# Kernel optimization log

Measured on AMD Instinct MI355X. Metric: run time of the kernel, lower is better.

The kernel has to match this reference:

```python
import jax, jax.numpy as jnp
import numpy as np

B, L, C, H = 4, 2048, 1024, 16
D = C // H            # head_dim = 64
HALF = D // 2         # 32
MAX_SCALE_MUL = float(np.log(100.0))


def setup_inputs() -> dict:
    key = jax.random.key(0)
    ks = jax.random.split(key, 6)
    x = jax.random.normal(ks[0], (B, L, C), dtype=jnp.float32)
    # causal additive bias [1,1,L,L]
    causal = jnp.tril(jnp.ones((L, L), dtype=bool))
    attn_bias = jnp.where(causal, 0.0, -1e9).astype(jnp.float32)[None, None]
    # RoPE cos/sin table: [B, 2, L, half]
    inv_freq = 1.0 / (10000.0 ** (jnp.arange(HALF, dtype=jnp.float32) / HALF))
    ang = jnp.arange(L, dtype=jnp.float32)[:, None] * inv_freq[None, :]  # [L, half]
    rope = jnp.stack([jnp.cos(ang), jnp.sin(ang)], axis=0)               # [2, L, half]
    rope_batch = jnp.broadcast_to(rope[None], (B, 2, L, HALF)).astype(jnp.float32)
    mat_qkv_w = jax.random.normal(ks[1], (3 * C, C), dtype=jnp.float32) * (1.0 / np.sqrt(C))
    q_bias = jnp.zeros((C,), dtype=jnp.float32)
    v_bias = jnp.zeros((C,), dtype=jnp.float32)
    proj_w = jax.random.normal(ks[2], (C, C), dtype=jnp.float32) * (1.0 / np.sqrt(C))
    proj_b = jnp.zeros((C,), dtype=jnp.float32)
    scale_mul = jnp.full((1, H, 1, 1), np.log(4.0), dtype=jnp.float32)
    return {"x": x, "attn_bias": attn_bias, "rope_batch": rope_batch,
            "mat_qkv_w": mat_qkv_w, "q_bias": q_bias, "v_bias": v_bias,
            "proj_w": proj_w, "proj_b": proj_b, "scale_mul": scale_mul}


def _l2norm(t, eps=1e-12):
    # F.normalize(t, dim=-1)
    n = jnp.sqrt(jnp.sum(t * t, axis=-1, keepdims=True))
    return t / jnp.maximum(n, eps)


def reference(x, attn_bias, rope_batch, mat_qkv_w, q_bias, v_bias, proj_w, proj_b, scale_mul):
    b, l, c = x.shape
    bias_cat = jnp.concatenate([q_bias, jnp.zeros_like(q_bias), v_bias])  # [3C]
    qkv = (x @ mat_qkv_w.T + bias_cat).reshape(b, l, 3, H, D)
    # non-flash layout: BHLc
    q = jnp.transpose(qkv[:, :, 0], (0, 2, 1, 3))
    k = jnp.transpose(qkv[:, :, 1], (0, 2, 1, 3))
    v = jnp.transpose(qkv[:, :, 2], (0, 2, 1, 3))
    # attn_l2_norm: scale=1, per-head learned multiplier
    sm = jnp.exp(jnp.minimum(scale_mul, MAX_SCALE_MUL))  # [1,H,1,1]
    q = _l2norm(q) * sm
    k = _l2norm(k)
    # RoPE (interleaved even/odd dims), start=0
    cos = rope_batch[:, 0, :l, :][:, None]  # [B,1,L,half]
    sin = rope_batch[:, 1, :l, :][:, None]
    def rot(t):
        t0, t1 = t[..., ::2], t[..., 1::2]
        r0 = t0 * cos - t1 * sin
        r1 = t0 * sin + t1 * cos
        return jnp.stack([r0, r1], axis=-1).reshape(t.shape)
    q, k = rot(q), rot(k)
    scale = 1.0  # attn_l2_norm path
    scores = jnp.einsum('bhqd,bhkd->bhqk', q, k) * scale + attn_bias
    attn = jax.nn.softmax(scores, axis=-1)
    out = jnp.einsum('bhqk,bhkd->bhqd', attn, v)
    out = jnp.transpose(out, (0, 2, 1, 3)).reshape(b, l, c)
    return out @ proj_w.T + proj_b
```

## Files before the change

kernel.cpp:

```cpp
#include <hip/hip_runtime.h>
#include <hip/hip_bf16.h>

#define BB 4
#define LL 2048
#define CC 1024
#define HH 16
#define DD 64
#define HALFD 32

typedef short bf16x8 __attribute__((ext_vector_type(8)));
typedef short bf16x4 __attribute__((ext_vector_type(4)));
typedef float f32x4 __attribute__((ext_vector_type(4)));

#if defined(__has_builtin)
#if __has_builtin(__builtin_amdgcn_mfma_f32_16x16x16bf16_1k)
#define HAVE_MFMA16 1
#endif
#endif

__device__ __forceinline__ float bf2f(unsigned short u) {
    union { unsigned int i; float f; } x; x.i = ((unsigned int)u) << 16; return x.f;
}
__device__ __forceinline__ unsigned short f2bf(float f) {
    union { float f; unsigned int i; } x; x.f = f;
    return (unsigned short)((x.i + 0x7fffu + ((x.i >> 16) & 1u)) >> 16);
}
__device__ __forceinline__ void gload_lds16(const void* g, void* l) {
    __builtin_amdgcn_global_load_lds(
        (const __attribute__((address_space(1))) unsigned int*)g,
        (__attribute__((address_space(3))) unsigned int*)l, 16, 0, 0);
}

__global__ void k_f2bf(const float4* __restrict__ in, ushort4* __restrict__ out, int n4) {
    int i = blockIdx.x * blockDim.x + threadIdx.x;
    if (i < n4) {
        float4 v = in[i];
        ushort4 o;
        o.x = f2bf(v.x); o.y = f2bf(v.y); o.z = f2bf(v.z); o.w = f2bf(v.w);
        out[i] = o;
    }
}

__global__ void k_biascat(const float* __restrict__ qb, const float* __restrict__ vb,
                          float* __restrict__ out) {
    int i = blockIdx.x * blockDim.x + threadIdx.x;
    if (i < 3 * CC) out[i] = (i < CC) ? qb[i] : (i < 2 * CC ? 0.f : vb[i - 2 * CC]);
}

template <typename OutT>
__global__ __launch_bounds__(256) void k_gemm_bt(
    const unsigned short* __restrict__ A, const unsigned short* __restrict__ Bt,
    const float* __restrict__ bias, OutT* __restrict__ Cout, int M, int N, int K) {
    __shared__ unsigned short As[128][32];
    __shared__ unsigned short Bs[128][32];
    int nT = N >> 7;
    int tM = (blockIdx.x / nT) << 7;
    int tN = (blockIdx.x % nT) << 7;
    int t = threadIdx.x;
    int lane = t & 63, wid = t >> 6;
    int wr = (wid >> 1) * 64, wc = (wid & 1) * 64;
    int c = lane & 15, g = lane >> 4;

    const unsigned short* gA = A + (size_t)(tM + wid * 32 + (lane >> 2)) * K + (lane & 3) * 8;
    const unsigned short* gB = Bt + (size_t)(tN + wid * 32 + (lane >> 2)) * K + (lane & 3) * 8;
    unsigned short* lA0 = &As[wid * 32][0];
    unsigned short* lA1 = &As[wid * 32 + 16][0];
    unsigned short* lB0 = &Bs[wid * 32][0];
    unsigned short* lB1 = &Bs[wid * 32 + 16][0];
    size_t r16 = (size_t)16 * K;

    f32x4 acc[4][4];
#pragma unroll
    for (int i = 0; i < 4; i++)
#pragma unroll
        for (int j = 0; j < 4; j++) acc[i][j] = (f32x4){0.f, 0.f, 0.f, 0.f};

    for (int k0 = 0; k0 < K; k0 += 32) {
        __syncthreads();
        gload_lds16(gA + k0, lA0);
        gload_lds16(gA + k0 + r16, lA1);
        gload_lds16(gB + k0, lB0);
        gload_lds16(gB + k0 + r16, lB1);
        __syncthreads();
        bf16x8 af[4], bfr[4];
#pragma unroll
        for (int fm = 0; fm < 4; fm++) af[fm] = *(const bf16x8*)&As[wr + fm * 16 + c][g * 8];
#pragma unroll
        for (int fn = 0; fn < 4; fn++) bfr[fn] = *(const bf16x8*)&Bs[wc + fn * 16 + c][g * 8];
#pragma unroll
        for (int fm = 0; fm < 4; fm++)
#pragma unroll
            for (int fn = 0; fn < 4; fn++)
                acc[fm][fn] = __builtin_amdgcn_mfma_f32_16x16x32_bf16(af[fm], bfr[fn],
                                                                      acc[fm][fn], 0, 0, 0);
    }
#pragma unroll
    for (int fm = 0; fm < 4; fm++) {
#pragma unroll
        for (int fn = 0; fn < 4; fn++) {
            int col = tN + wc + fn * 16 + c;
            float bv = bias[col];
#pragma unroll
            for (int r = 0; r < 4; r++) {
                int row = tM + wr + fm * 16 + g * 4 + r;
                float v = acc[fm][fn][r] + bv;
                if constexpr (sizeof(OutT) == 2)
                    Cout[(size_t)row * N + col] = f2bf(v);
                else
                    Cout[(size_t)row * N + col] = v;
            }
        }
    }
}

__global__ __launch_bounds__(256) void k_qknorm(
    const unsigned short* __restrict__ qkv, const float* __restrict__ rope,
    const float* __restrict__ smul, unsigned short* __restrict__ Q,
    unsigned short* __restrict__ Ko) {
    int wid = threadIdx.x >> 6, lane = threadIdx.x & 63;
    long rowid = (long)blockIdx.x * 4 + wid;
    int h = rowid & 15;
    long t2 = rowid >> 4;
    int l = t2 & 2047;
    int b = (int)(t2 >> 11);
    size_t base = ((size_t)(b * LL + l) * 3) * CC + h * 64 + lane;
    float q = bf2f(qkv[base]);
    float k = bf2f(qkv[base + CC]);
    float sq = q * q, sk = k * k;
#pragma unroll
    for (int m = 32; m >= 1; m >>= 1) {
        sq += __shfl_xor(sq, m);
        sk += __shfl_xor(sk, m);
    }
    float sm = expf(fminf(smul[h], 4.6051701859880913680f));
    q = q / fmaxf(sqrtf(sq), 1e-12f) * sm;
    k = k / fmaxf(sqrtf(sk), 1e-12f);
    int j = lane >> 1;
    float cs = rope[((size_t)(b * 2) * LL + l) * HALFD + j];
    float sn = rope[((size_t)(b * 2 + 1) * LL + l) * HALFD + j];
    float qp = __shfl_xor(q, 1), kp = __shfl_xor(k, 1);
    float qn = (lane & 1) ? (qp * sn + q * cs) : (q * cs - qp * sn);
    float kn = (lane & 1) ? (kp * sn + k * cs) : (k * cs - kp * sn);
    size_t ob = ((size_t)(b * HH + h) * LL + l) * 64 + lane;
    Q[ob] = f2bf(qn);
    Ko[ob] = f2bf(kn);
}

__global__ __launch_bounds__(256) void k_vtrans(const unsigned short* __restrict__ qkv,
                                               unsigned short* __restrict__ Vt) {
    __shared__ unsigned short tile[64][65];
    int bid = blockIdx.x;
    int lb = bid & 31;
    int bh = bid >> 5;
    int h = bh & 15, b = bh >> 4;
    int t = threadIdx.x;
    for (int i = t; i < 4096; i += 256) {
        int row = i >> 6, dd = i & 63;
        tile[row][dd] = qkv[((size_t)(b * LL + lb * 64 + row) * 3 + 2) * CC + h * 64 + dd];
    }
    __syncthreads();
    for (int i = t; i < 4096; i += 256) {
        int dd = i >> 6, l2 = i & 63;
        Vt[((size_t)bh * 64 + dd) * LL + lb * 64 + l2] = tile[l2][dd];
    }
}

__global__ __launch_bounds__(256) void k_attn(
    const unsigned short* __restrict__ Q, const unsigned short* __restrict__ K,
    const unsigned short* __restrict__ Vt, unsigned short* __restrict__ Out) {
    int lane = threadIdx.x & 63, wid = threadIdx.x >> 6;
    int c = lane & 15, g = lane >> 4;
    int bid = blockIdx.x;
    int bh = bid & 63;
    int strip = 15 - (bid >> 6);
    int qb = strip * 128 + wid * 32;
    const unsigned short* Qh = Q + (size_t)bh * LL * 64;
    const unsigned short* Kh = K + (size_t)bh * LL * 64;
    const unsigned short* Vh = Vt + (size_t)bh * 64 * LL;

    bf16x8 qf[2][2];
#pragma unroll
    for (int qt = 0; qt < 2; qt++)
#pragma unroll
        for (int ch = 0; ch < 2; ch++)
            qf[qt][ch] =
                *(const bf16x8*)&Qh[(size_t)(qb + qt * 16 + c) * 64 + ch * 32 + g * 8];

    f32x4 acc[2][4];
#pragma unroll
    for (int qt = 0; qt < 2; qt++)
#pragma unroll
        for (int dt = 0; dt < 4; dt++) acc[qt][dt] = (f32x4){0.f, 0.f, 0.f, 0.f};
    float m_[2] = {-1e30f, -1e30f}, l_[2] = {0.f, 0.f};

#ifndef HAVE_MFMA16
    int srcA = 32 * (g & 1) + c;
    int srcB = srcA + 16;
#endif

    for (int kt = 0; kt < qb + 32; kt += 64) {
        bf16x8 kf[4][2];
#pragma unroll
        for (int kt2 = 0; kt2 < 4; kt2++)
#pragma unroll
            for (int ch = 0; ch < 2; ch++)
                kf[kt2][ch] =
                    *(const bf16x8*)&Kh[(size_t)(kt + kt2 * 16 + c) * 64 + ch * 32 + g * 8];
#ifdef HAVE_MFMA16
        bf16x4 vf[4][4];
#pragma unroll
        for (int dt = 0; dt < 4; dt++)
#pragma unroll
            for (int kt2 = 0; kt2 < 4; kt2++)
                vf[dt][kt2] =
                    *(const bf16x4*)&Vh[(size_t)(dt * 16 + c) * LL + kt + kt2 * 16 + 4 * g];
#else
        bf16x8 vf8[4][2];
#pragma unroll
        for (int dt = 0; dt < 4; dt++)
#pragma unroll
            for (int hf = 0; hf < 2; hf++)
                vf8[dt][hf] =
                    *(const bf16x8*)&Vh[(size_t)(dt * 16 + c) * LL + kt + hf * 32 + 8 * g];
#endif
#pragma unroll
        for (int qt = 0; qt < 2; qt++) {
            int qtb = qb + qt * 16;
            int qrow = qtb + c;
            f32x4 s[4];
#pragma unroll
            for (int kt2 = 0; kt2 < 4; kt2++) {
                s[kt2] = (f32x4){0.f, 0.f, 0.f, 0.f};
                s[kt2] = __builtin_amdgcn_mfma_f32_16x16x32_bf16(kf[kt2][0], qf[qt][0],
                                                                 s[kt2], 0, 0, 0);
                s[kt2] = __builtin_amdgcn_mfma_f32_16x16x32_bf16(kf[kt2][1], qf[qt][1],
                                                                 s[kt2], 0, 0, 0);
            }
            if (kt + 63 > qtb) {
#pragma unroll
                for (int kt2 = 0; kt2 < 4; kt2++) {
                    if (kt + kt2 * 16 + 15 > qtb) {
#pragma unroll
                        for (int r = 0; r < 4; r++)
                            if (kt + kt2 * 16 + 4 * g + r > qrow) s[kt2][r] = -1e9f;
                    }
                }
            }
            float tm = fmaxf(fmaxf(fmaxf(s[0][0], s[0][1]), fmaxf(s[0][2], s[0][3])),
                             fmaxf(fmaxf(s[1][0], s[1][1]), fmaxf(s[1][2], s[1][3])));
            float tm2 = fmaxf(fmaxf(fmaxf(s[2][0], s[2][1]), fmaxf(s[2][2], s[2][3])),
                              fmaxf(fmaxf(s[3][0], s[3][1]), fmaxf(s[3][2], s[3][3])));
            tm = fmaxf(tm, tm2);
            tm = fmaxf(tm, __shfl_xor(tm, 16));
            tm = fmaxf(tm, __shfl_xor(tm, 32));
            if (__any(tm > m_[qt] + 8.0f)) {
                float mn = fmaxf(m_[qt], tm);
                float scl = __expf(m_[qt] - mn);
                m_[qt] = mn;
                l_[qt] *= scl;
#pragma unroll
                for (int dt = 0; dt < 4; dt++) {
                    acc[qt][dt][0] *= scl; acc[qt][dt][1] *= scl;
                    acc[qt][dt][2] *= scl; acc[qt][dt][3] *= scl;
                }
            }
            float p[4][4];
            float rs = 0.f;
#pragma unroll
            for (int kt2 = 0; kt2 < 4; kt2++)
#pragma unroll
                for (int r = 0; r < 4; r++) {
                    p[kt2][r] = __expf(s[kt2][r] - m_[qt]);
                    rs += p[kt2][r];
                }
            rs += __shfl_xor(rs, 16);
            rs += __shfl_xor(rs, 32);
            l_[qt] += rs;
#ifdef HAVE_MFMA16
            bf16x4 pb[4];
#pragma unroll
            for (int kt2 = 0; kt2 < 4; kt2++)
#pragma unroll
                for (int r = 0; r < 4; r++) pb[kt2][r] = (short)f2bf(p[kt2][r]);
#pragma unroll
            for (int dt = 0; dt < 4; dt++)
#pragma unroll
                for (int kt2 = 0; kt2 < 4; kt2++)
                    acc[qt][dt] = __builtin_amdgcn_mfma_f32_16x16x16bf16_1k(
                        vf[dt][kt2], pb[kt2], acc[qt][dt], 0, 0, 0);
#else
#pragma unroll
            for (int hf = 0; hf < 2; hf++) {
                unsigned int A0 = (unsigned int)f2bf(p[2 * hf][0]) |
                                  ((unsigned int)f2bf(p[2 * hf][1]) << 16);
                unsigned int A1 = (unsigned int)f2bf(p[2 * hf][2]) |
                                  ((unsigned int)f2bf(p[2 * hf][3]) << 16);
                unsigned int B0 = (unsigned int)f2bf(p[2 * hf + 1][0]) |
                                  ((unsigned int)f2bf(p[2 * hf + 1][1]) << 16);
                unsigned int B1 = (unsigned int)f2bf(p[2 * hf + 1][2]) |
                                  ((unsigned int)f2bf(p[2 * hf + 1][3]) << 16);
                int t0a = __shfl((int)A0, srcA), t0b = __shfl((int)B0, srcA);
                int t1a = __shfl((int)A1, srcA), t1b = __shfl((int)B1, srcA);
                int t2a = __shfl((int)A0, srcB), t2b = __shfl((int)B0, srcB);
                int t3a = __shfl((int)A1, srcB), t3b = __shfl((int)B1, srcB);
                union { int w[4]; bf16x8 v; } u;
                bool hi = (g & 2) != 0;
                u.w[0] = hi ? t0b : t0a;
                u.w[1] = hi ? t1b : t1a;
                u.w[2] = hi ? t2b : t2a;
                u.w[3] = hi ? t3b : t3a;
#pragma unroll
                for (int dt = 0; dt < 4; dt++)
                    acc[qt][dt] = __builtin_amdgcn_mfma_f32_16x16x32_bf16(
                        vf8[dt][hf], u.v, acc[qt][dt], 0, 0, 0);
            }
#endif
        }
    }
    int b = bh >> 4, h = bh & 15;
#pragma unroll
    for (int qt = 0; qt < 2; qt++) {
        float inv = 1.f / l_[qt];
        int qg = qb + qt * 16 + c;
        size_t ob = ((size_t)b * LL + qg) * CC + h * 64;
#pragma unroll
        for (int dt = 0; dt < 4; dt++) {
            ushort4 o;
            o.x = f2bf(acc[qt][dt][0] * inv);
            o.y = f2bf(acc[qt][dt][1] * inv);
            o.z = f2bf(acc[qt][dt][2] * inv);
            o.w = f2bf(acc[qt][dt][3] * inv);
            *(ushort4*)&Out[ob + dt * 16 + 4 * g] = o;
        }
    }
}

extern "C" void kernel_launch(void* const* d_in, const int* in_sizes, int n_in,
                              void* d_out, int out_size, void* d_ws, size_t ws_size,
                              hipStream_t stream) {
    const float* x = (const float*)d_in[0];
    const float* rope = (const float*)d_in[2];
    const float* w1 = (const float*)d_in[3];
    const float* qb = (const float*)d_in[4];
    const float* vb = (const float*)d_in[5];
    const float* w2 = (const float*)d_in[6];
    const float* pb = (const float*)d_in[7];
    const float* smul = (const float*)d_in[8];
    float* out = (float*)d_out;

    char* ws = (char*)d_ws;
    unsigned short* xb = (unsigned short*)(ws + 0);
    unsigned short* w1b = (unsigned short*)(ws + 16777216);
    unsigned short* w2b = (unsigned short*)(ws + 23068672);
    float* biascat = (float*)(ws + 25165824);
    unsigned short* qkvb = (unsigned short*)(ws + 25178112);
    unsigned short* Qb = (unsigned short*)(ws + 75509760);
    unsigned short* Kb = (unsigned short*)(ws + 92286976);
    unsigned short* Vtb = (unsigned short*)(ws + 109064192);
    unsigned short* attb = (unsigned short*)(ws + 125841408);
    if (ws_size < 142618624) return;

    int n4;
    n4 = BB * LL * CC / 4;
    k_f2bf<<<(n4 + 255) / 256, 256, 0, stream>>>((const float4*)x, (ushort4*)xb, n4);
    n4 = 3 * CC * CC / 4;
    k_f2bf<<<(n4 + 255) / 256, 256, 0, stream>>>((const float4*)w1, (ushort4*)w1b, n4);
    n4 = CC * CC / 4;
    k_f2bf<<<(n4 + 255) / 256, 256, 0, stream>>>((const float4*)w2, (ushort4*)w2b, n4);
    k_biascat<<<12, 256, 0, stream>>>(qb, vb, biascat);

    k_gemm_bt<unsigned short><<<(8192 / 128) * (3072 / 128), 256, 0, stream>>>(
        xb, w1b, biascat, qkvb, BB * LL, 3 * CC, CC);

    k_qknorm<<<BB * LL * HH / 4, 256, 0, stream>>>(qkvb, rope, smul, Qb, Kb);
    k_vtrans<<<BB * HH * (LL / 64), 256, 0, stream>>>(qkvb, Vtb);
    k_attn<<<64 * 16, 256, 0, stream>>>(Qb, Kb, Vtb, attb);

    k_gemm_bt<float><<<(8192 / 128) * (1024 / 128), 256, 0, stream>>>(
        attb, w2b, pb, out, BB * LL, CC, CC);
}
```

Before: 347.8 us.

## Tune attention kernel with exp2 softmax, packed bf16 converts, XCD-aware mapping

Folds log2(e) into the per-head q scale so the softmax can use the raw v_exp_f32 (exp2) instruction, and replaces the manual bf16 rounding with the hardware v_cvt_pk_bf16_f32 packed convert. The block-to-(head, query strip) mapping is reordered so consecutive blocks on the same XCD share a head, which should improve L2 reuse of K/V. Workgroup-uniform key loop bounds with per-query-tile skipping, s_setprio around the MFMA sections, and a raised rescale threshold (12 in log2 units) are added. Together these target cheaper exp and convert work and better cache locality, at the cost of slightly different rounding behaviour.

```diff
diff --git a/kernel.cpp b/kernel.cpp
--- a/kernel.cpp
+++ b/kernel.cpp
@@ -24,6 +24,16 @@
 __device__ __forceinline__ unsigned short f2bf(float f) {
     union { float f; unsigned int i; } x; x.f = f;
     return (unsigned short)((x.i + 0x7fffu + ((x.i >> 16) & 1u)) >> 16);
+}
+__device__ __forceinline__ unsigned int cvtpk_bf16(float lo, float hi) {
+    unsigned int r;
+    asm("v_cvt_pk_bf16_f32 %0, %1, %2" : "=v"(r) : "v"(lo), "v"(hi));
+    return r;
+}
+__device__ __forceinline__ float exp2v(float x) {
+    float r;
+    asm("v_exp_f32 %0, %1" : "=v"(r) : "v"(x));
+    return r;
 }
 __device__ __forceinline__ void gload_lds16(const void* g, void* l) {
     __builtin_amdgcn_global_load_lds(
@@ -132,7 +142,7 @@
         sq += __shfl_xor(sq, m);
         sk += __shfl_xor(sk, m);
     }
-    float sm = expf(fminf(smul[h], 4.6051701859880913680f));
+    float sm = expf(fminf(smul[h], 4.6051701859880913680f)) * 1.4426950408889634f;
     q = q / fmaxf(sqrtf(sq), 1e-12f) * sm;
     k = k / fmaxf(sqrtf(sk), 1e-12f);
     int j = lane >> 1;
@@ -171,9 +181,13 @@
     int lane = threadIdx.x & 63, wid = threadIdx.x >> 6;
     int c = lane & 15, g = lane >> 4;
     int bid = blockIdx.x;
-    int bh = bid & 63;
-    int strip = 15 - (bid >> 6);
-    int qb = strip * 128 + wid * 32;
+    int xcd = bid & 7;
+    int idx = bid >> 3;
+    int qblk = 15 - (idx & 15);
+    int hgrp = idx >> 4;
+    int bh = hgrp * 8 + xcd;
+    int qb0 = qblk * 128;
+    int qb = qb0 + wid * 32;
     const unsigned short* Qh = Q + (size_t)bh * LL * 64;
     const unsigned short* Kh = K + (size_t)bh * LL * 64;
     const unsigned short* Vh = Vt + (size_t)bh * 64 * LL;
@@ -198,7 +212,7 @@
     int srcB = srcA + 16;
 #endif
 
-    for (int kt = 0; kt < qb + 32; kt += 64) {
+    for (int kt = 0; kt < qb0 + 128; kt += 64) {
         bf16x8 kf[4][2];
 #pragma unroll
         for (int kt2 = 0; kt2 < 4; kt2++)
@@ -226,8 +240,10 @@
 #pragma unroll
         for (int qt = 0; qt < 2; qt++) {
             int qtb = qb + qt * 16;
+            if (kt > qtb + 15) continue;
             int qrow = qtb + c;
             f32x4 s[4];
+            __builtin_amdgcn_s_setprio(1);
 #pragma unroll
             for (int kt2 = 0; kt2 < 4; kt2++) {
                 s[kt2] = (f32x4){0.f, 0.f, 0.f, 0.f};
@@ -236,6 +252,7 @@
                 s[kt2] = __builtin_amdgcn_mfma_f32_16x16x32_bf16(kf[kt2][1], qf[qt][1],
                                                                  s[kt2], 0, 0, 0);
             }
+            __builtin_amdgcn_s_setprio(0);
             if (kt + 63 > qtb) {
 #pragma unroll
                 for (int kt2 = 0; kt2 < 4; kt2++) {
@@ -253,9 +270,9 @@
             tm = fmaxf(tm, tm2);
             tm = fmaxf(tm, __shfl_xor(tm, 16));
             tm = fmaxf(tm, __shfl_xor(tm, 32));
-            if (__any(tm > m_[qt] + 8.0f)) {
+            if (__any(tm > m_[qt] + 12.0f)) {
                 float mn = fmaxf(m_[qt], tm);
-                float scl = __expf(m_[qt] - mn);
+                float scl = exp2v(m_[qt] - mn);
                 m_[qt] = mn;
                 l_[qt] *= scl;
 #pragma unroll
@@ -270,7 +287,7 @@
             for (int kt2 = 0; kt2 < 4; kt2++)
 #pragma unroll
                 for (int r = 0; r < 4; r++) {
-                    p[kt2][r] = __expf(s[kt2][r] - m_[qt]);
+                    p[kt2][r] = exp2v(s[kt2][r] - m_[qt]);
                     rs += p[kt2][r];
                 }
             rs += __shfl_xor(rs, 16);
@@ -279,26 +296,27 @@
 #ifdef HAVE_MFMA16
             bf16x4 pb[4];
 #pragma unroll
-            for (int kt2 = 0; kt2 < 4; kt2++)
-#pragma unroll
-                for (int r = 0; r < 4; r++) pb[kt2][r] = (short)f2bf(p[kt2][r]);
+            for (int kt2 = 0; kt2 < 4; kt2++) {
+                union { unsigned int w[2]; bf16x4 v; } pu;
+                pu.w[0] = cvtpk_bf16(p[kt2][0], p[kt2][1]);
+                pu.w[1] = cvtpk_bf16(p[kt2][2], p[kt2][3]);
+                pb[kt2] = pu.v;
+            }
+            __builtin_amdgcn_s_setprio(1);
 #pragma unroll
             for (int dt = 0; dt < 4; dt++)
 #pragma unroll
                 for (int kt2 = 0; kt2 < 4; kt2++)
                     acc[qt][dt] = __builtin_amdgcn_mfma_f32_16x16x16bf16_1k(
                         vf[dt][kt2], pb[kt2], acc[qt][dt], 0, 0, 0);
+            __builtin_amdgcn_s_setprio(0);
 #else
 #pragma unroll
             for (int hf = 0; hf < 2; hf++) {
-                unsigned int A0 = (unsigned int)f2bf(p[2 * hf][0]) |
-                                  ((unsigned int)f2bf(p[2 * hf][1]) << 16);
-                unsigned int A1 = (unsigned int)f2bf(p[2 * hf][2]) |
-                                  ((unsigned int)f2bf(p[2 * hf][3]) << 16);
-                unsigned int B0 = (unsigned int)f2bf(p[2 * hf + 1][0]) |
-                                  ((unsigned int)f2bf(p[2 * hf + 1][1]) << 16);
-                unsigned int B1 = (unsigned int)f2bf(p[2 * hf + 1][2]) |
-                                  ((unsigned int)f2bf(p[2 * hf + 1][3]) << 16);
+                unsigned int A0 = cvtpk_bf16(p[2 * hf][0], p[2 * hf][1]);
+                unsigned int A1 = cvtpk_bf16(p[2 * hf][2], p[2 * hf][3]);
+                unsigned int B0 = cvtpk_bf16(p[2 * hf + 1][0], p[2 * hf + 1][1]);
+                unsigned int B1 = cvtpk_bf16(p[2 * hf + 1][2], p[2 * hf + 1][3]);
                 int t0a = __shfl((int)A0, srcA), t0b = __shfl((int)B0, srcA);
                 int t1a = __shfl((int)A1, srcA), t1b = __shfl((int)B1, srcA);
                 int t2a = __shfl((int)A0, srcB), t2b = __shfl((int)B0, srcB);
@@ -325,12 +343,10 @@
         size_t ob = ((size_t)b * LL + qg) * CC + h * 64;
 #pragma unroll
         for (int dt = 0; dt < 4; dt++) {
-            ushort4 o;
-            o.x = f2bf(acc[qt][dt][0] * inv);
-            o.y = f2bf(acc[qt][dt][1] * inv);
-            o.z = f2bf(acc[qt][dt][2] * inv);
-            o.w = f2bf(acc[qt][dt][3] * inv);
-            *(ushort4*)&Out[ob + dt * 16 + 4 * g] = o;
+            union { unsigned int w[2]; ushort4 v; } o;
+            o.w[0] = cvtpk_bf16(acc[qt][dt][0] * inv, acc[qt][dt][1] * inv);
+            o.w[1] = cvtpk_bf16(acc[qt][dt][2] * inv, acc[qt][dt][3] * inv);
+            *(ushort4*)&Out[ob + dt * 16 + 4 * g] = o.v;
         }
     }
 }
@@ -374,7 +390,7 @@
 
     k_qknorm<<<BB * LL * HH / 4, 256, 0, stream>>>(qkvb, rope, smul, Qb, Kb);
     k_vtrans<<<BB * HH * (LL / 64), 256, 0, stream>>>(qkvb, Vtb);
-    k_attn<<<64 * 16, 256, 0, stream>>>(Qb, Kb, Vtb, attb);
+    k_attn<<<1024, 256, 0, stream>>>(Qb, Kb, Vtb, attb);
 
     k_gemm_bt<float><<<(8192 / 128) * (1024 / 128), 256, 0, stream>>>(
         attb, w2b, pb, out, BB * LL, CC, CC);
```

After: 408.9 us. 1.18x slower.
